# Optimization experiments

Hardware: AMD Instinct MI355X
Metric: run time of the kernel (lower is better)

## Reference

```python
import jax, jax.numpy as jnp
import numpy as np

B, IN, H = 8192, 1024, 1024

def _ln(x, g, b, eps=1e-5):
    mu = jnp.mean(x, axis=-1, keepdims=True)
    var = jnp.mean(jnp.square(x - mu), axis=-1, keepdims=True)
    return (x - mu) * jax.lax.rsqrt(var + eps) * g + b

def setup_inputs() -> dict:
    key = jax.random.key(0)
    ks = jax.random.split(key, 8)
    s_h = 1.0 / np.sqrt(H)
    s_i = 1.0 / np.sqrt(IN)
    inp = {
        'x': jax.random.normal(ks[0], (B, IN), jnp.float32),
        'h': jax.random.normal(ks[1], (B, H), jnp.float32),
        'W_r': jax.random.uniform(ks[2], (H, H), jnp.float32, -s_h, s_h),
        'U_r': jax.random.uniform(ks[3], (H, IN), jnp.float32, -s_i, s_i),
        'W_u': jax.random.uniform(ks[4], (H, H), jnp.float32, -s_h, s_h),
        'U_u': jax.random.uniform(ks[5], (H, IN), jnp.float32, -s_i, s_i),
        'W_c': jax.random.uniform(ks[6], (H, H), jnp.float32, -s_h, s_h),
        'U_c': jax.random.uniform(ks[7], (H, IN), jnp.float32, -s_i, s_i),
        # LayerNorm params: rows = [r_hidden, r_input, u_hidden, u_input, c_hidden, c_input]
        'ln_gamma': 0.1 * jnp.ones((6, H), jnp.float32),
        'ln_beta': jnp.zeros((6, H), jnp.float32),
    }
    return inp

def reference(x, h, W_r, U_r, W_u, U_u, W_c, U_c, ln_gamma, ln_beta):
    g, b = ln_gamma, ln_beta
    # nn.Linear(bias=False): y = x @ W.T
    r = jax.nn.sigmoid(_ln(h @ W_r.T, g[0], b[0]) + _ln(x @ U_r.T, g[1], b[1]))
    u = jax.nn.sigmoid(_ln(h @ W_u.T, g[2], b[2]) + _ln(x @ U_u.T, g[3], b[3]))
    c = jnp.tanh(_ln((h * r) @ W_c.T, g[4], b[4]) + _ln(x @ U_c.T, g[5], b[5]))
    return (1.0 - u) * h + u * c
```

## Files before the change

kernel.cpp:

```cpp
#include <hip/hip_runtime.h>
#include <cstdint>
#include <cstddef>

typedef unsigned short u16;
typedef unsigned char u8;
typedef __attribute__((ext_vector_type(8))) short bf16x8;
typedef __attribute__((ext_vector_type(4))) float f32x4;
typedef __attribute__((ext_vector_type(4))) int i32x4;
typedef __attribute__((ext_vector_type(8))) int i32x8;

__device__ inline float bf2f(u16 u) { return __uint_as_float(((unsigned)u) << 16); }
__device__ inline unsigned f2bf(float f) {
  unsigned u = __float_as_uint(f);
  u += 0x7fffu + ((u >> 16) & 1u);
  return u >> 16;
}

__device__ inline unsigned f2fp8(float f) {
  unsigned s = (__float_as_uint(f) >> 31) << 7;
  float a = fabsf(f);
  if (a >= 0.015625f) {
    unsigned u = __float_as_uint(a);
    u += 0x7FFFFu + ((u >> 20) & 1u);
    unsigned e = (u >> 23) - 120u;
    unsigned m = (u >> 20) & 7u;
    return s | (e << 3) | m;
  }
  int m = (int)rintf(a * 512.0f);
  return s | (unsigned)m;
}

__device__ inline void async16(const void* g, void* l) {
  __builtin_amdgcn_global_load_lds(
      (const __attribute__((address_space(1))) void*)g,
      (__attribute__((address_space(3))) void*)l, 16, 0, 0);
}

__device__ inline i32x8 join8(i32x4 lo, i32x4 hi) {
  i32x8 r;
  r[0] = lo[0]; r[1] = lo[1]; r[2] = lo[2]; r[3] = lo[3];
  r[4] = hi[0]; r[5] = hi[1]; r[6] = hi[2]; r[7] = hi[3];
  return r;
}

__device__ inline void unpack8(uint4 q, float* o) {
  o[0] = bf2f((u16)(q.x & 0xffffu)); o[1] = bf2f((u16)(q.x >> 16));
  o[2] = bf2f((u16)(q.y & 0xffffu)); o[3] = bf2f((u16)(q.y >> 16));
  o[4] = bf2f((u16)(q.z & 0xffffu)); o[5] = bf2f((u16)(q.z >> 16));
  o[6] = bf2f((u16)(q.w & 0xffffu)); o[7] = bf2f((u16)(q.w >> 16));
}

__device__ inline uint4 pack8(const float* v) {
  uint4 q;
  q.x = f2bf(v[0]) | (f2bf(v[1]) << 16);
  q.y = f2bf(v[2]) | (f2bf(v[3]) << 16);
  q.z = f2bf(v[4]) | (f2bf(v[5]) << 16);
  q.w = f2bf(v[6]) | (f2bf(v[7]) << 16);
  return q;
}

__device__ inline float fast_sigmoid(float z) {
  return 1.0f / (1.0f + exp2f(-1.4426950408889634f * z));
}
__device__ inline float fast_tanh(float z) {
  return 1.0f - 2.0f / (1.0f + exp2f(2.8853900817779268f * z));
}

struct ConvArgs2 {
  const float* x; const float* h; const float* wr; const float* ur;
  const float* wbf[4];
  u16* xb; u16* hb; u8* x8; u8* h8; u8* w8r; u8* w8u;
  u16* wbo[4];
};

__global__ __launch_bounds__(256) void convert_all(ConvArgs2 a) {
  const int b = blockIdx.x;
  const int t = threadIdx.x;
  if (b < 16384) {
    const bool isx = b < 8192;
    const int off = isx ? b : b - 8192;
    const float* __restrict__ s = isx ? a.x : a.h;
    u16* __restrict__ db = isx ? a.xb : a.hb;
    u8*  __restrict__ d8 = isx ? a.x8 : a.h8;
    const int i = (off * 256 + t) * 4;
    float4 v = *(const float4*)(s + i);
    uint2 o;
    o.x = f2bf(v.x) | (f2bf(v.y) << 16);
    o.y = f2bf(v.z) | (f2bf(v.w) << 16);
    *(uint2*)(db + i) = o;
    unsigned q = f2fp8(v.x) | (f2fp8(v.y) << 8) | (f2fp8(v.z) << 16) | (f2fp8(v.w) << 24);
    *(unsigned*)(d8 + i) = q;
  } else if (b < 18432) {
    const bool isr = b < 17408;
    const int off = isr ? b - 16384 : b - 17408;
    const float* __restrict__ s = isr ? a.wr : a.ur;
    u8* __restrict__ d8 = isr ? a.w8r : a.w8u;
    const int i = (off * 256 + t) * 4;
    float4 v = *(const float4*)(s + i);
    unsigned q = f2fp8(v.x * 8192.f) | (f2fp8(v.y * 8192.f) << 8) |
                 (f2fp8(v.z * 8192.f) << 16) | (f2fp8(v.w * 8192.f) << 24);
    *(unsigned*)(d8 + i) = q;
  } else {
    const int tt = b - 18432;
    const int which = tt >> 10;
    const int off = tt & 1023;
    const float* __restrict__ s = a.wbf[which];
    u16* __restrict__ d = a.wbo[which];
    const int i = (off * 256 + t) * 4;
    float4 v = *(const float4*)(s + i);
    uint2 o;
    o.x = f2bf(v.x) | (f2bf(v.y) << 16);
    o.y = f2bf(v.z) | (f2bf(v.w) << 16);
    *(uint2*)(d + i) = o;
  }
}

struct GemmF8 { const u8* A[2]; const u8* Bw[2]; u16* Y[2]; };

__global__ __launch_bounds__(256) void gemm_fp8(GemmF8 args) {
  const int p = blockIdx.x;
  const int xcd = p & 7;
  const int s = p >> 3;
  const int pr = s >> 4;
  const int cc = s & 15;
  const int gate = cc >> 3;
  const int col = cc & 7;
  const int r = pr * 8 + xcd;

  const u8* __restrict__ A  = args.A[gate];
  const u8* __restrict__ Bw = args.Bw[gate];
  u16* __restrict__ Y = args.Y[gate];

  __shared__ __attribute__((aligned(16))) u8 As[128 * 128];
  __shared__ __attribute__((aligned(16))) u8 Bs[128 * 128];

  const int tid  = threadIdx.x;
  const int lane = tid & 63;
  const int w    = tid >> 6;
  const int wm   = w >> 1;
  const int wn   = w & 1;

  const int rowBlk = r * 128;
  const int colBlk = col * 128;

  const int srow = lane >> 3;
  const int scol = ((lane & 7) ^ srow) * 16;
  const u8* gA[4]; const u8* gB[4]; u8* lA[4]; u8* lB[4];
#pragma unroll
  for (int i = 0; i < 4; i++) {
    const int rr = w * 32 + i * 8;
    gA[i] = A  + (size_t)(rowBlk + rr + srow) * 1024 + scol;
    gB[i] = Bw + (size_t)(colBlk + rr + srow) * 1024 + scol;
    lA[i] = &As[rr * 128];
    lB[i] = &Bs[rr * 128];
  }

  const int sw = lane & 7;
  const int g0 = (lane >> 4) * 2;
  const int o0 = ((g0 ^ sw) << 4);
  const int o1 = (((g0 + 1) ^ sw) << 4);
  const int frA = (wm * 64 + (lane & 15)) * 128;
  const int frB = (wn * 64 + (lane & 15)) * 128;

  f32x4 acc[4][4] = {};

  for (int k0 = 0; k0 < 1024; k0 += 128) {
#pragma unroll
    for (int i = 0; i < 4; i++) {
      async16(gA[i] + k0, lA[i]);
      async16(gB[i] + k0, lB[i]);
    }
    __syncthreads();
    i32x8 af[4], bfr[4];
#pragma unroll
    for (int t = 0; t < 4; t++) {
      const int ra = frA + t * 16 * 128;
      const int rb = frB + t * 16 * 128;
      af[t]  = join8(*(const i32x4*)&As[ra + o0], *(const i32x4*)&As[ra + o1]);
      bfr[t] = join8(*(const i32x4*)&Bs[rb + o0], *(const i32x4*)&Bs[rb + o1]);
    }
#pragma unroll
    for (int tm = 0; tm < 4; tm++)
#pragma unroll
      for (int tn = 0; tn < 4; tn++)
        acc[tm][tn] = __builtin_amdgcn_mfma_scale_f32_16x16x128_f8f6f4(
            af[tm], bfr[tn], acc[tm][tn],
            0, 0,
            0, 127,
            0, 114);
    __syncthreads();
  }

  const int rBase = rowBlk + wm * 64 + (lane >> 4) * 4;
  const int cBase = colBlk + wn * 64 + (lane & 15);
#pragma unroll
  for (int tm = 0; tm < 4; tm++) {
#pragma unroll
    for (int i = 0; i < 4; i++) {
      const size_t rr = (size_t)(rBase + tm * 16 + i);
#pragma unroll
      for (int tn = 0; tn < 4; tn++)
        Y[rr * 1024 + cBase + tn * 16] = (u16)f2bf(acc[tm][tn][i]);
    }
  }
}

struct Gemm4 { const u16* A[4]; const u16* Bw[4]; u16* Y[4]; };

template <int NG_LOG2>
__global__ __launch_bounds__(256) void gemm_batch(Gemm4 args) {
  const int p = blockIdx.x;
  const int xcd = p & 7;
  const int s = p >> 3;
  const int pr = s >> (3 + NG_LOG2);
  const int cc = s & ((8 << NG_LOG2) - 1);
  const int gate = cc >> 3;
  const int col  = cc & 7;
  const int r = pr * 8 + xcd;

  const u16* __restrict__ A  = args.A[gate];
  const u16* __restrict__ Bw = args.Bw[gate];
  u16* __restrict__ Y = args.Y[gate];

  __shared__ __attribute__((aligned(16))) u16 As[128 * 64];
  __shared__ __attribute__((aligned(16))) u16 Bs[128 * 64];

  const int tid  = threadIdx.x;
  const int lane = tid & 63;
  const int w    = tid >> 6;
  const int wm   = w >> 1;
  const int wn   = w & 1;

  const int rowBlk = r * 128;
  const int colBlk = col * 128;

  const int srow = lane >> 3;
  const int scol = ((lane & 7) ^ srow) * 8;
  const u16* gA[4]; const u16* gB[4]; u16* lA[4]; u16* lB[4];
#pragma unroll
  for (int i = 0; i < 4; i++) {
    const int rr = w * 32 + i * 8;
    gA[i] = A  + (size_t)(rowBlk + rr + srow) * 1024 + scol;
    gB[i] = Bw + (size_t)(colBlk + rr + srow) * 1024 + scol;
    lA[i] = &As[rr * 64];
    lB[i] = &Bs[rr * 64];
  }

  const int swz = (((lane >> 4) ^ (lane & 7)) << 3);
  const int fa = (wm * 64 + (lane & 15)) * 64 + swz;
  const int fb = (wn * 64 + (lane & 15)) * 64 + swz;

  f32x4 acc[4][4] = {};

  for (int k0 = 0; k0 < 1024; k0 += 64) {
#pragma unroll
    for (int i = 0; i < 4; i++) {
      async16(gA[i] + k0, lA[i]);
      async16(gB[i] + k0, lB[i]);
    }
    __syncthreads();
#pragma unroll
    for (int kk = 0; kk < 2; kk++) {
      const int kx = kk << 5;
      bf16x8 af[4], bfr[4];
#pragma unroll
      for (int t = 0; t < 4; t++) {
        af[t]  = *(const bf16x8*)&As[(fa + t * 1024) ^ kx];
        bfr[t] = *(const bf16x8*)&Bs[(fb + t * 1024) ^ kx];
      }
#pragma unroll
      for (int tm = 0; tm < 4; tm++)
#pragma unroll
        for (int tn = 0; tn < 4; tn++)
          acc[tm][tn] = __builtin_amdgcn_mfma_f32_16x16x32_bf16(af[tm], bfr[tn], acc[tm][tn], 0, 0, 0);
    }
    __syncthreads();
  }

  const int rBase = rowBlk + wm * 64 + (lane >> 4) * 4;
  const int cBase = colBlk + wn * 64 + (lane & 15);
#pragma unroll
  for (int tm = 0; tm < 4; tm++) {
#pragma unroll
    for (int i = 0; i < 4; i++) {
      const size_t rr = (size_t)(rBase + tm * 16 + i);
#pragma unroll
      for (int tn = 0; tn < 4; tn++)
        Y[rr * 1024 + cBase + tn * 16] = (u16)f2bf(acc[tm][tn][i]);
    }
  }
}

__global__ __launch_bounds__(256) void rgate_kernel(
    const u16* __restrict__ Yrh, const u16* __restrict__ Yrx,
    const u16* __restrict__ hb, const float* __restrict__ gamma,
    const float* __restrict__ beta, u16* __restrict__ hrb) {
  const int row  = blockIdx.x * 4 + (threadIdx.x >> 6);
  const int lane = threadIdx.x & 63;
  const size_t rb = (size_t)row * 1024;

  uint4 qa[2], qb[2], qh[2];
  qa[0] = *(const uint4*)(Yrh + rb + lane * 8);
  qa[1] = *(const uint4*)(Yrh + rb + 512 + lane * 8);
  qb[0] = *(const uint4*)(Yrx + rb + lane * 8);
  qb[1] = *(const uint4*)(Yrx + rb + 512 + lane * 8);
  qh[0] = *(const uint4*)(hb  + rb + lane * 8);
  qh[1] = *(const uint4*)(hb  + rb + 512 + lane * 8);

  float s0 = 0.f, s0q = 0.f, s1 = 0.f, s1q = 0.f;
  float tmp[8];
#pragma unroll
  for (int c = 0; c < 2; c++) {
    unpack8(qa[c], tmp);
#pragma unroll
    for (int j = 0; j < 8; j++) { s0 += tmp[j]; s0q += tmp[j] * tmp[j]; }
    unpack8(qb[c], tmp);
#pragma unroll
    for (int j = 0; j < 8; j++) { s1 += tmp[j]; s1q += tmp[j] * tmp[j]; }
  }
#pragma unroll
  for (int off = 1; off < 64; off <<= 1) {
    s0 += __shfl_xor(s0, off, 64);  s0q += __shfl_xor(s0q, off, 64);
    s1 += __shfl_xor(s1, off, 64);  s1q += __shfl_xor(s1q, off, 64);
  }

  const float inv = 1.0f / 1024.0f;
  const float mu0 = s0 * inv, rs0 = rsqrtf(s0q * inv - mu0 * mu0 + 1e-5f);
  const float mu1 = s1 * inv, rs1 = rsqrtf(s1q * inv - mu1 * mu1 + 1e-5f);

#pragma unroll
  for (int c = 0; c < 2; c++) {
    const int cb = c * 512 + lane * 8;
    float va[8], vb[8], vh[8], o[8];
    unpack8(qa[c], va); unpack8(qb[c], vb); unpack8(qh[c], vh);
#pragma unroll
    for (int j = 0; j < 8; j++) {
      const float ln0 = (va[j] - mu0) * rs0 * gamma[cb + j] + beta[cb + j];
      const float ln1 = (vb[j] - mu1) * rs1 * gamma[1024 + cb + j] + beta[1024 + cb + j];
      const float rg = fast_sigmoid(ln0 + ln1);
      o[j] = vh[j] * rg;
    }
    *(uint4*)(hrb + rb + cb) = pack8(o);
  }
}

__global__ __launch_bounds__(256) void final_fuse(
    const u16* __restrict__ Yuh, const u16* __restrict__ Yux,
    const u16* __restrict__ Ych, const u16* __restrict__ Ycx,
    const float* __restrict__ h, const float* __restrict__ gamma,
    const float* __restrict__ beta, float* __restrict__ out) {
  const int row  = blockIdx.x * 4 + (threadIdx.x >> 6);
  const int lane = threadIdx.x & 63;
  const size_t rb = (size_t)row * 1024;

  uint4 q0[2], q1[2], q2[2], q3[2];
  float4 hf[4];
#pragma unroll
  for (int c = 0; c < 2; c++) {
    const int cb = c * 512 + lane * 8;
    q0[c] = *(const uint4*)(Yuh + rb + cb);
    q1[c] = *(const uint4*)(Yux + rb + cb);
    q2[c] = *(const uint4*)(Ych + rb + cb);
    q3[c] = *(const uint4*)(Ycx + rb + cb);
    hf[c * 2]     = *(const float4*)(h + rb + cb);
    hf[c * 2 + 1] = *(const float4*)(h + rb + cb + 4);
  }

  float s[8] = {0.f, 0.f, 0.f, 0.f, 0.f, 0.f, 0.f, 0.f};
  float tmp[8];
#pragma unroll
  for (int c = 0; c < 2; c++) {
    unpack8(q0[c], tmp);
#pragma unroll
    for (int j = 0; j < 8; j++) { s[0] += tmp[j]; s[1] += tmp[j] * tmp[j]; }
    unpack8(q1[c], tmp);
#pragma unroll
    for (int j = 0; j < 8; j++) { s[2] += tmp[j]; s[3] += tmp[j] * tmp[j]; }
    unpack8(q2[c], tmp);
#pragma unroll
    for (int j = 0; j < 8; j++) { s[4] += tmp[j]; s[5] += tmp[j] * tmp[j]; }
    unpack8(q3[c], tmp);
#pragma unroll
    for (int j = 0; j < 8; j++) { s[6] += tmp[j]; s[7] += tmp[j] * tmp[j]; }
  }
#pragma unroll
  for (int off = 1; off < 64; off <<= 1) {
#pragma unroll
    for (int q = 0; q < 8; q++) s[q] += __shfl_xor(s[q], off, 64);
  }

  const float inv = 1.0f / 1024.0f;
  const float mu0 = s[0] * inv, rs0 = rsqrtf(s[1] * inv - mu0 * mu0 + 1e-5f);
  const float mu1 = s[2] * inv, rs1 = rsqrtf(s[3] * inv - mu1 * mu1 + 1e-5f);
  const float mu2 = s[4] * inv, rs2 = rsqrtf(s[5] * inv - mu2 * mu2 + 1e-5f);
  const float mu3 = s[6] * inv, rs3 = rsqrtf(s[7] * inv - mu3 * mu3 + 1e-5f);

#pragma unroll
  for (int c = 0; c < 2; c++) {
    const int cb = c * 512 + lane * 8;
    float v0[8], v1[8], v2[8], v3[8];
    unpack8(q0[c], v0); unpack8(q1[c], v1); unpack8(q2[c], v2); unpack8(q3[c], v3);
    const float* hv = (const float*)&hf[c * 2];
    float o[8];
#pragma unroll
    for (int j = 0; j < 8; j++) {
      const int cc = cb + j;
      const float ln2 = (v0[j] - mu0) * rs0 * gamma[2 * 1024 + cc] + beta[2 * 1024 + cc];
      const float ln3 = (v1[j] - mu1) * rs1 * gamma[3 * 1024 + cc] + beta[3 * 1024 + cc];
      const float ln4 = (v2[j] - mu2) * rs2 * gamma[4 * 1024 + cc] + beta[4 * 1024 + cc];
      const float ln5 = (v3[j] - mu3) * rs3 * gamma[5 * 1024 + cc] + beta[5 * 1024 + cc];
      const float u  = fast_sigmoid(ln2 + ln3);
      const float cg = fast_tanh(ln4 + ln5);
      o[j] = (1.0f - u) * hv[j] + u * cg;
    }
    *(float4*)(out + rb + cb)     = *(float4*)&o[0];
    *(float4*)(out + rb + cb + 4) = *(float4*)&o[4];
  }
}

extern "C" void kernel_launch(void* const* d_in, const int* in_sizes, int n_in,
                              void* d_out, int out_size, void* d_ws, size_t ws_size,
                              hipStream_t stream) {
  const float* x  = (const float*)d_in[0];
  const float* h  = (const float*)d_in[1];
  const float* W_r = (const float*)d_in[2];
  const float* U_r = (const float*)d_in[3];
  const float* W_u = (const float*)d_in[4];
  const float* U_u = (const float*)d_in[5];
  const float* W_c = (const float*)d_in[6];
  const float* U_c = (const float*)d_in[7];
  const float* gamma = (const float*)d_in[8];
  const float* beta  = (const float*)d_in[9];
  float* out = (float*)d_out;

  char* ws = (char*)d_ws;
  const size_t MB = 1024 * 1024;
  const size_t SZ_ACT = 16 * MB;

  u16* xb = (u16*)(ws);
  u16* hb = (u16*)(ws + 16 * MB);
  u16* wb[4];
  for (int i = 0; i < 4; i++) wb[i] = (u16*)(ws + (32 + 2 * i) * MB);
  u8* w8r = (u8*)(ws + 40 * MB);
  u8* w8u = (u8*)(ws + 41 * MB);
  char* ybase = ws + 42 * MB;
  u16* Y0 = (u16*)(ybase);
  u16* Y1 = (u16*)(ybase + SZ_ACT);
  u16* Y2 = (u16*)(ybase + 2 * SZ_ACT);
  u16* Y3 = (u16*)(ybase + 3 * SZ_ACT);
  u16* Y5 = (u16*)(ybase + 4 * SZ_ACT);
  u8* x8 = (u8*)Y5;
  u8* h8 = (u8*)Y5 + 8 * MB;

  ConvArgs2 ca = {};
  ca.x = x; ca.h = h; ca.wr = W_r; ca.ur = U_r;
  ca.wbf[0] = W_u; ca.wbf[1] = U_u; ca.wbf[2] = W_c; ca.wbf[3] = U_c;
  ca.xb = xb; ca.hb = hb; ca.x8 = x8; ca.h8 = h8; ca.w8r = w8r; ca.w8u = w8u;
  ca.wbo[0] = (u16*)(ws + 32 * MB); ca.wbo[1] = (u16*)(ws + 34 * MB);
  ca.wbo[2] = (u16*)(ws + 36 * MB); ca.wbo[3] = (u16*)(ws + 38 * MB);
  convert_all<<<22528, 256, 0, stream>>>(ca);

  GemmF8 gf = {};
  gf.A[0] = h8; gf.Bw[0] = w8r; gf.Y[0] = Y0;
  gf.A[1] = x8; gf.Bw[1] = w8u; gf.Y[1] = Y1;
  gemm_fp8<<<1024, 256, 0, stream>>>(gf);

  rgate_kernel<<<2048, 256, 0, stream>>>(Y0, Y1, hb, gamma, beta, Y1);

  Gemm4 gb = {};
  gb.A[0] = xb; gb.Bw[0] = wb[1]; gb.Y[0] = Y3;
  gb.A[1] = xb; gb.Bw[1] = wb[3]; gb.Y[1] = Y5;
  gb.A[2] = hb; gb.Bw[2] = wb[0]; gb.Y[2] = Y2;
  gb.A[3] = Y1; gb.Bw[3] = wb[2]; gb.Y[3] = Y0;
  gemm_batch<2><<<2048, 256, 0, stream>>>(gb);

  final_fuse<<<2048, 256, 0, stream>>>(Y2, Y3, Y0, Y5, h, gamma, beta, out);
}
```

Before: 285.5 us.

## Replace batched bf16 GEMM with 256x256-tile double-buffered 8-wave pipelined kernel

Replaces the 128x128-tile, 4-wave batched GEMM, which does a single-buffered load-then-compute per k step, with a 256x256-tile kernel using 8 waves and double-buffered LDS (128 KB). Global-to-LDS async loads for the next k tiles are split into phases and interleaved with MFMA sub-blocks. Explicit barriers, waitcnt and setprio keep copies in flight while compute runs. The larger tiles raise data reuse per byte loaded, at the cost of higher register and LDS pressure and a fragile hand-tuned synchronization schedule.

```diff
diff --git a/kernel.cpp b/kernel.cpp
--- a/kernel.cpp
+++ b/kernel.cpp
@@ -207,86 +207,142 @@
 
 struct Gemm4 { const u16* A[4]; const u16* Bw[4]; u16* Y[4]; };
 
-template <int NG_LOG2>
-__global__ __launch_bounds__(256) void gemm_batch(Gemm4 args) {
+__global__ __launch_bounds__(512, 2) void gemm_8ph(Gemm4 args) {
   const int p = blockIdx.x;
-  const int xcd = p & 7;
-  const int s = p >> 3;
-  const int pr = s >> (3 + NG_LOG2);
-  const int cc = s & ((8 << NG_LOG2) - 1);
-  const int gate = cc >> 3;
-  const int col  = cc & 7;
-  const int r = pr * 8 + xcd;
+  const int wg = (p & 7) * 64 + (p >> 3);
+  const int gate = wg >> 7;
+  const int rem  = wg & 127;
+  const int rblk = rem >> 2;
+  const int cblk = rem & 3;
 
   const u16* __restrict__ A  = args.A[gate];
   const u16* __restrict__ Bw = args.Bw[gate];
   u16* __restrict__ Y = args.Y[gate];
 
-  __shared__ __attribute__((aligned(16))) u16 As[128 * 64];
-  __shared__ __attribute__((aligned(16))) u16 Bs[128 * 64];
+  __shared__ __attribute__((aligned(16))) u16 sm[2][2][2][128 * 64];
 
   const int tid  = threadIdx.x;
   const int lane = tid & 63;
   const int w    = tid >> 6;
-  const int wm   = w >> 1;
-  const int wn   = w & 1;
-
-  const int rowBlk = r * 128;
-  const int colBlk = col * 128;
-
-  const int srow = lane >> 3;
-  const int scol = ((lane & 7) ^ srow) * 8;
-  const u16* gA[4]; const u16* gB[4]; u16* lA[4]; u16* lB[4];
-#pragma unroll
-  for (int i = 0; i < 4; i++) {
-    const int rr = w * 32 + i * 8;
-    gA[i] = A  + (size_t)(rowBlk + rr + srow) * 1024 + scol;
-    gB[i] = Bw + (size_t)(colBlk + rr + srow) * 1024 + scol;
-    lA[i] = &As[rr * 64];
-    lB[i] = &Bs[rr * 64];
-  }
-
-  const int swz = (((lane >> 4) ^ (lane & 7)) << 3);
-  const int fa = (wm * 64 + (lane & 15)) * 64 + swz;
-  const int fb = (wn * 64 + (lane & 15)) * 64 + swz;
-
-  f32x4 acc[4][4] = {};
-
-  for (int k0 = 0; k0 < 1024; k0 += 64) {
-#pragma unroll
-    for (int i = 0; i < 4; i++) {
-      async16(gA[i] + k0, lA[i]);
-      async16(gB[i] + k0, lB[i]);
-    }
-    __syncthreads();
-#pragma unroll
-    for (int kk = 0; kk < 2; kk++) {
-      const int kx = kk << 5;
-      bf16x8 af[4], bfr[4];
-#pragma unroll
-      for (int t = 0; t < 4; t++) {
-        af[t]  = *(const bf16x8*)&As[(fa + t * 1024) ^ kx];
-        bfr[t] = *(const bf16x8*)&Bs[(fb + t * 1024) ^ kx];
+  const int wm   = w >> 2;
+  const int wn   = w & 3;
+
+  const int l8   = lane >> 3;
+  const int sgrp = (lane & 7) ^ l8;
+  const u16* aSrc = A  + ((size_t)(rblk * 256 + w * 8 + l8) << 10) + sgrp * 8;
+  const u16* bSrc = Bw + ((size_t)(cblk * 256 + w * 8 + l8) << 10) + sgrp * 8;
+  const int ldsW = w * 8 * 64;
+
+  const int fr = (lane & 15) * 64 + ((((lane >> 4) ^ (lane & 7))) << 3);
+
+  f32x4 acc_lo[4][4] = {};
+  f32x4 acc_hi[4][4] = {};
+
+  auto stage = [&](const u16* src, int tt, int op, int half) {
+    const int d = tt & 1;
+    const u16* s = src + (size_t)half * 131072 + tt * 64;
+    u16* l0 = &sm[d][op][half][ldsW];
+    async16(s, l0);
+    async16(s + 65536, l0 + 4096);
+  };
+
+  stage(bSrc, 0, 1, 0); stage(bSrc, 0, 1, 1);
+  stage(aSrc, 0, 0, 0); stage(aSrc, 0, 0, 1);
+  stage(bSrc, 1, 1, 0); stage(bSrc, 1, 1, 1);
+  stage(aSrc, 1, 0, 0);
+  asm volatile("s_waitcnt vmcnt(6)" ::: "memory");
+  __builtin_amdgcn_s_barrier();
+
+  for (int t = 0; t < 16; ++t) {
+    const int d = t & 1;
+    const u16* baseA = &sm[d][0][wm][0];
+    const u16* baseB = &sm[d][1][wn >> 1][(wn & 1) * 4096];
+
+    bf16x8 alo[2][4], bfg[2][4];
+#pragma unroll
+    for (int kk = 0; kk < 2; ++kk) {
+      const int fo = fr ^ (kk << 5);
+#pragma unroll
+      for (int m = 0; m < 4; ++m) alo[kk][m] = *(const bf16x8*)(baseA + m * 1024 + fo);
+#pragma unroll
+      for (int n = 0; n < 4; ++n) bfg[kk][n] = *(const bf16x8*)(baseB + n * 1024 + fo);
+    }
+    if (t + 1 < 16) stage(aSrc, t + 1, 0, 1);
+    __builtin_amdgcn_s_barrier();
+    asm volatile("s_waitcnt lgkmcnt(0)" ::: "memory");
+    __builtin_amdgcn_s_setprio(1);
+#pragma unroll
+    for (int m = 0; m < 4; ++m)
+#pragma unroll
+      for (int n = 0; n < 2; ++n)
+#pragma unroll
+        for (int kk = 0; kk < 2; ++kk)
+          acc_lo[m][n] = __builtin_amdgcn_mfma_f32_16x16x32_bf16(alo[kk][m], bfg[kk][n], acc_lo[m][n], 0, 0, 0);
+    __builtin_amdgcn_s_setprio(0);
+    __builtin_amdgcn_s_barrier();
+
+    if (t + 2 < 16) stage(bSrc, t + 2, 1, 0);
+    __builtin_amdgcn_s_barrier();
+    __builtin_amdgcn_s_setprio(1);
+#pragma unroll
+    for (int m = 0; m < 4; ++m)
+#pragma unroll
+      for (int n = 2; n < 4; ++n)
+#pragma unroll
+        for (int kk = 0; kk < 2; ++kk)
+          acc_lo[m][n] = __builtin_amdgcn_mfma_f32_16x16x32_bf16(alo[kk][m], bfg[kk][n], acc_lo[m][n], 0, 0, 0);
+    __builtin_amdgcn_s_setprio(0);
+    __builtin_amdgcn_s_barrier();
+
+    bf16x8 ahi[2][4];
+#pragma unroll
+    for (int kk = 0; kk < 2; ++kk) {
+      const int fo = fr ^ (kk << 5);
+#pragma unroll
+      for (int m = 0; m < 4; ++m) ahi[kk][m] = *(const bf16x8*)(baseA + (m + 4) * 1024 + fo);
+    }
+    if (t + 2 < 16) stage(bSrc, t + 2, 1, 1);
+    __builtin_amdgcn_s_barrier();
+    asm volatile("s_waitcnt lgkmcnt(0)" ::: "memory");
+    __builtin_amdgcn_s_setprio(1);
+#pragma unroll
+    for (int m = 0; m < 4; ++m)
+#pragma unroll
+      for (int n = 0; n < 2; ++n)
+#pragma unroll
+        for (int kk = 0; kk < 2; ++kk)
+          acc_hi[m][n] = __builtin_amdgcn_mfma_f32_16x16x32_bf16(ahi[kk][m], bfg[kk][n], acc_hi[m][n], 0, 0, 0);
+    __builtin_amdgcn_s_setprio(0);
+    __builtin_amdgcn_s_barrier();
+
+    if (t + 2 < 16) stage(aSrc, t + 2, 0, 0);
+    __builtin_amdgcn_s_barrier();
+    __builtin_amdgcn_s_setprio(1);
+#pragma unroll
+    for (int m = 0; m < 4; ++m)
+#pragma unroll
+      for (int n = 2; n < 4; ++n)
+#pragma unroll
+        for (int kk = 0; kk < 2; ++kk)
+          acc_hi[m][n] = __builtin_amdgcn_mfma_f32_16x16x32_bf16(ahi[kk][m], bfg[kk][n], acc_hi[m][n], 0, 0, 0);
+    __builtin_amdgcn_s_setprio(0);
+    if (t < 14) asm volatile("s_waitcnt vmcnt(6)" ::: "memory");
+    else        asm volatile("s_waitcnt vmcnt(0)" ::: "memory");
+    __builtin_amdgcn_s_barrier();
+  }
+
+  const int rBase = rblk * 256 + wm * 128 + (lane >> 4) * 4;
+  const int cBase = cblk * 256 + wn * 64 + (lane & 15);
+#pragma unroll
+  for (int m = 0; m < 4; ++m) {
+#pragma unroll
+    for (int i = 0; i < 4; ++i) {
+      const size_t r0 = (size_t)(rBase + m * 16 + i) * 1024 + cBase;
+#pragma unroll
+      for (int n = 0; n < 4; ++n) {
+        Y[r0 + n * 16]             = (u16)f2bf(acc_lo[m][n][i]);
+        Y[r0 + 64 * 1024 + n * 16] = (u16)f2bf(acc_hi[m][n][i]);
       }
-#pragma unroll
-      for (int tm = 0; tm < 4; tm++)
-#pragma unroll
-        for (int tn = 0; tn < 4; tn++)
-          acc[tm][tn] = __builtin_amdgcn_mfma_f32_16x16x32_bf16(af[tm], bfr[tn], acc[tm][tn], 0, 0, 0);
-    }
-    __syncthreads();
-  }
-
-  const int rBase = rowBlk + wm * 64 + (lane >> 4) * 4;
-  const int cBase = colBlk + wn * 64 + (lane & 15);
-#pragma unroll
-  for (int tm = 0; tm < 4; tm++) {
-#pragma unroll
-    for (int i = 0; i < 4; i++) {
-      const size_t rr = (size_t)(rBase + tm * 16 + i);
-#pragma unroll
-      for (int tn = 0; tn < 4; tn++)
-        Y[rr * 1024 + cBase + tn * 16] = (u16)f2bf(acc[tm][tn][i]);
     }
   }
 }
@@ -472,7 +528,7 @@
   gb.A[1] = xb; gb.Bw[1] = wb[3]; gb.Y[1] = Y5;
   gb.A[2] = hb; gb.Bw[2] = wb[0]; gb.Y[2] = Y2;
   gb.A[3] = Y1; gb.Bw[3] = wb[2]; gb.Y[3] = Y0;
-  gemm_batch<2><<<2048, 256, 0, stream>>>(gb);
+  gemm_8ph<<<512, 512, 0, stream>>>(gb);
 
   final_fuse<<<2048, 256, 0, stream>>>(Y2, Y3, Y0, Y5, h, gamma, beta, out);
 }
```

Result: faster. 270.9 us (-5.1%).
